# Performance work log

Measured on AMD Instinct MI355X. Metric: run time of the kernel, lower is better.

Reference implementation:

```python
import jax, jax.numpy as jnp
import numpy as np

B, S, D, H, DFF = 8, 1024, 1024, 16, 4096
DK = D // H
EPS = 1e-5


def setup_inputs() -> dict:
    key = jax.random.key(0)
    ks = jax.random.split(key, 12)
    sc = lambda n: 1.0 / np.sqrt(n)
    return {
        "x": jax.random.normal(ks[0], (B, S, D), jnp.float32),
        "src_mask": jnp.ones((B, 1, 1, S), jnp.int32),
        "wq": jax.random.normal(ks[1], (D, D), jnp.float32) * sc(D),
        "bq": jnp.zeros((D,), jnp.float32),
        "wk": jax.random.normal(ks[2], (D, D), jnp.float32) * sc(D),
        "bk": jnp.zeros((D,), jnp.float32),
        "wv": jax.random.normal(ks[3], (D, D), jnp.float32) * sc(D),
        "bv": jnp.zeros((D,), jnp.float32),
        "wo": jax.random.normal(ks[4], (D, D), jnp.float32) * sc(D),
        "bo": jnp.zeros((D,), jnp.float32),
        "w1": jax.random.normal(ks[5], (DFF, D), jnp.float32) * sc(D),
        "b1": jnp.zeros((DFF,), jnp.float32),
        "w2": jax.random.normal(ks[6], (D, DFF), jnp.float32) * sc(DFF),
        "b2": jnp.zeros((D,), jnp.float32),
        "g1": jnp.ones((1,), jnp.float32),
        "be1": jnp.zeros((1,), jnp.float32),
        "g2": jnp.ones((1,), jnp.float32),
        "be2": jnp.zeros((1,), jnp.float32),
    }


def _layernorm(x, gamma, beta):
    # Faithful to source: torch.var defaults to unbiased (ddof=1); scalar gamma/beta.
    mu = jnp.mean(x, axis=-1, keepdims=True)
    var = jnp.var(x, axis=-1, keepdims=True, ddof=1)
    return gamma * (x - mu) / jnp.sqrt(var + EPS) + beta


def _mha(x, wq, bq, wk, bk, wv, bv, wo, bo):
    q = (x @ wq.T + bq).reshape(B, S, H, DK).transpose(0, 2, 1, 3)
    k = (x @ wk.T + bk).reshape(B, S, H, DK).transpose(0, 2, 1, 3)
    v = (x @ wv.T + bv).reshape(B, S, H, DK).transpose(0, 2, 1, 3)
    scores = jnp.einsum("bhqd,bhkd->bhqk", q, k) / np.sqrt(DK)
    # NOTE: source uses non-inplace masked_fill whose result is discarded,
    # so the mask has no effect on the executed math; we replicate that.
    attn = jax.nn.softmax(scores, axis=-1)
    out = jnp.einsum("bhqk,bhkd->bhqd", attn, v)
    out = out.transpose(0, 2, 1, 3).reshape(B, S, D)
    return out @ wo.T + bo


def reference(x, src_mask, wq, bq, wk, bk, wv, bv, wo, bo,
              w1, b1, w2, b2, g1, be1, g2, be2):
    # residual 1: pre-norm self-attention (dropout=0 in eval)
    x = x + _mha(_layernorm(x, g1, be1), wq, bq, wk, bk, wv, bv, wo, bo)
    # residual 2: pre-norm FFN
    h = _layernorm(x, g2, be2)
    ff = jax.nn.relu(h @ w1.T + b1) @ w2.T + b2
    return x + ff
```

## Files before the change

kernel.cpp:

```cpp
#include <hip/hip_runtime.h>

typedef unsigned short u16;
typedef unsigned int u32;
typedef __attribute__((ext_vector_type(8))) __bf16 bf16x8;
typedef __attribute__((ext_vector_type(4))) float f32x4;

#define B_ 8
#define S_ 1024
#define D_ 1024
#define H_ 16
#define DK_ 64
#define DFF_ 4096
#define LDQKV 3072

__device__ __forceinline__ float bflo(u32 u) { return __uint_as_float(u << 16); }
__device__ __forceinline__ float bfhi(u32 u) { return __uint_as_float(u & 0xffff0000u); }
__device__ __forceinline__ u16 f2bf(float f) {
    u32 u = __float_as_uint(f);
    u += 0x7fffu + ((u >> 16) & 1u);
    return (u16)(u >> 16);
}

__device__ __forceinline__ void gl2lds16(const u16* g, u16* l) {
    __builtin_amdgcn_global_load_lds(
        (const __attribute__((address_space(1))) void*)g,
        (__attribute__((address_space(3))) void*)l, 16, 0, 0);
}

__global__ __launch_bounds__(256) void sniff_kernel(const u16* __restrict__ w,
                                                    int* __restrict__ flag) {
    float mx = 0.f;
    for (int i = threadIdx.x; i < 4096; i += 256) {
        float v = fabsf(bflo((u32)w[i]));
        if (!isnan(v)) mx = fmaxf(mx, v);
    }
#pragma unroll
    for (int m = 1; m < 64; m <<= 1) mx = fmaxf(mx, __shfl_xor(mx, m, 64));
    __shared__ float wmx[4];
    if ((threadIdx.x & 63) == 0) wmx[threadIdx.x >> 6] = mx;
    __syncthreads();
    if (threadIdx.x == 0) {
        float m2 = fmaxf(fmaxf(wmx[0], wmx[1]), fmaxf(wmx[2], wmx[3]));
        *flag = (m2 > 1e3f) ? 1 : 0;
    }
}

__global__ __launch_bounds__(256) void norm_kernel(const void* __restrict__ in,
                                                   u16* __restrict__ out, int n,
                                                   const int* __restrict__ flag) {
    const int i = blockIdx.x * 256 + threadIdx.x;
    if (i >= n) return;
    if (*flag)
        out[i] = f2bf(((const float*)in)[i]);
    else
        out[i] = ((const u16*)in)[i];
}

struct SmallTbl {
    const void* src[10];
    u16* dst[10];
    int n[10];
};
__global__ __launch_bounds__(256) void norm_small(SmallTbl tb,
                                                  const int* __restrict__ flag) {
    int i = blockIdx.x * 256 + threadIdx.x;
    const int f = *flag;
#pragma unroll
    for (int j = 0; j < 10; ++j) {
        if (i < tb.n[j]) {
            if (f)
                tb.dst[j][i] = f2bf(((const float*)tb.src[j])[i]);
            else
                tb.dst[j][i] = ((const u16*)tb.src[j])[i];
            return;
        }
        i -= tb.n[j];
    }
}

template <int INF32>
__global__ __launch_bounds__(256) void ln_kernel(const void* __restrict__ in,
                                                 const u16* __restrict__ gs,
                                                 const u16* __restrict__ bs,
                                                 u16* __restrict__ out) {
    const int row = blockIdx.x, t = threadIdx.x;
    float v0, v1, v2, v3;
    if (INF32) {
        const float* p = (const float*)in + (size_t)row * D_ + t * 4;
        float4 f = *(const float4*)p;
        v0 = f.x; v1 = f.y; v2 = f.z; v3 = f.w;
    } else {
        const u16* p = (const u16*)in + (size_t)row * D_ + t * 4;
        uint2 u = *(const uint2*)p;
        v0 = bflo(u.x); v1 = bfhi(u.x); v2 = bflo(u.y); v3 = bfhi(u.y);
    }
    float s = v0 + v1 + v2 + v3;
    float sq = v0 * v0 + v1 * v1 + v2 * v2 + v3 * v3;
#pragma unroll
    for (int m = 1; m < 64; m <<= 1) {
        s += __shfl_xor(s, m, 64);
        sq += __shfl_xor(sq, m, 64);
    }
    __shared__ float ss[4], sqs[4];
    const int w = t >> 6;
    if ((t & 63) == 0) { ss[w] = s; sqs[w] = sq; }
    __syncthreads();
    s = ss[0] + ss[1] + ss[2] + ss[3];
    sq = sqs[0] + sqs[1] + sqs[2] + sqs[3];
    const float mu = s * (1.f / 1024.f);
    float var = (sq - 1024.f * mu * mu) * (1.f / 1023.f);
    var = fmaxf(var, 0.f);
    const float rstd = rsqrtf(var + 1e-5f);
    const float gm = bflo((u32)gs[0]);
    const float bt = bflo((u32)bs[0]);
    const float y0 = gm * (v0 - mu) * rstd + bt;
    const float y1 = gm * (v1 - mu) * rstd + bt;
    const float y2 = gm * (v2 - mu) * rstd + bt;
    const float y3 = gm * (v3 - mu) * rstd + bt;
    uint2 uo;
    uo.x = (u32)f2bf(y0) | ((u32)f2bf(y1) << 16);
    uo.y = (u32)f2bf(y2) | ((u32)f2bf(y3) << 16);
    *(uint2*)(out + (size_t)row * D_ + t * 4) = uo;
}

template <int RELU, int RES, int OUTF>
__global__ __launch_bounds__(256, 2) void gemm_bt(const u16* __restrict__ A,
                                                  const u16* __restrict__ W,
                                                  const u16* __restrict__ bias,
                                                  const void* __restrict__ res,
                                                  void* __restrict__ out,
                                                  int M, int N, int K,
                                                  const int* __restrict__ oflag) {
    __shared__ __align__(16) u16 As[128 * 32];
    __shared__ __align__(16) u16 Bs[128 * 32];
    const int t = threadIdx.x;
    const int lane = t & 63, w = t >> 6;
    const int wm = w >> 1, wn = w & 1;
    const int m0 = blockIdx.y * 128, n0 = blockIdx.x * 128;

    f32x4 acc[4][4];
#pragma unroll
    for (int mi = 0; mi < 4; ++mi)
#pragma unroll
        for (int ni = 0; ni < 4; ++ni) acc[mi][ni] = (f32x4){0.f, 0.f, 0.f, 0.f};

    const int sr = lane >> 2, skc = lane & 3;
    const u16* Ag0 = A + (size_t)(m0 + w * 16 + sr) * K + skc * 8;
    const u16* Bg0 = W + (size_t)(n0 + w * 16 + sr) * K + skc * 8;
    const size_t h64 = (size_t)64 * K;
    u16* Asd0 = &As[(w * 16) * 32];
    u16* Asd1 = &As[(64 + w * 16) * 32];
    u16* Bsd0 = &Bs[(w * 16) * 32];
    u16* Bsd1 = &Bs[(64 + w * 16) * 32];

    const u16* As_r = &As[(wm * 64 + (lane & 15)) * 32 + (lane >> 4) * 8];
    const u16* Bs_r = &Bs[(wn * 64 + (lane & 15)) * 32 + (lane >> 4) * 8];

    for (int kt = 0; kt < K; kt += 32) {
        __syncthreads();
        gl2lds16(Ag0 + kt, Asd0);
        gl2lds16(Ag0 + h64 + kt, Asd1);
        gl2lds16(Bg0 + kt, Bsd0);
        gl2lds16(Bg0 + h64 + kt, Bsd1);
        __syncthreads();
        bf16x8 af[4], bfr[4];
#pragma unroll
        for (int i = 0; i < 4; ++i) {
            af[i] = *(const bf16x8*)(As_r + i * 16 * 32);
            bfr[i] = *(const bf16x8*)(Bs_r + i * 16 * 32);
        }
#pragma unroll
        for (int mi = 0; mi < 4; ++mi)
#pragma unroll
            for (int ni = 0; ni < 4; ++ni)
                acc[mi][ni] = __builtin_amdgcn_mfma_f32_16x16x32_bf16(af[mi], bfr[ni], acc[mi][ni], 0, 0, 0);
    }

    const bool f32o = (OUTF == 1) || (OUTF == 2 && oflag[0] != 0);
    const int qd = lane >> 4, cl = lane & 15;
#pragma unroll
    for (int ni = 0; ni < 4; ++ni) {
        const int col = n0 + wn * 64 + ni * 16 + cl;
        const float bv = bflo((u32)bias[col]);
#pragma unroll
        for (int mi = 0; mi < 4; ++mi) {
#pragma unroll
            for (int j = 0; j < 4; ++j) {
                const int row = m0 + wm * 64 + mi * 16 + qd * 4 + j;
                float vv = acc[mi][ni][j] + bv;
                if (RELU) vv = fmaxf(vv, 0.f);
                if (RES == 1) vv += bflo((u32)((const u16*)res)[(size_t)row * N + col]);
                if (RES == 2) vv += ((const float*)res)[(size_t)row * N + col];
                if (f32o)
                    ((float*)out)[(size_t)row * N + col] = vv;
                else
                    ((u16*)out)[(size_t)row * N + col] = f2bf(vv);
            }
        }
    }
}

__global__ __launch_bounds__(256, 2) void attn_mfma(const u16* __restrict__ QKV,
                                                    u16* __restrict__ O) {
    __shared__ __align__(16) u16 lds[6 * 64 * 72];
    u16* Ks = lds;
    u16* VsT = lds + 64 * 72;

    const int t = threadIdx.x;
    const int lane = t & 63, w = t >> 6;
    u16* Pw = lds + (2 + w) * 64 * 72;
    const int b = blockIdx.y >> 4, h = blockIdx.y & 15;
    const int q_base = blockIdx.x * 256 + w * 64;
    const int c = lane & 15, g = lane >> 4;
    const float SC = 0.18033688011112042f;

    bf16x8 qfrag[4][2];
#pragma unroll
    for (int ni = 0; ni < 4; ++ni)
#pragma unroll
        for (int kc = 0; kc < 2; ++kc)
            qfrag[ni][kc] = *(const bf16x8*)(QKV + (size_t)(b * S_ + q_base + 16 * ni + c) * LDQKV +
                                             h * 64 + kc * 32 + 8 * g);

    f32x4 acc_o[4][4];
#pragma unroll
    for (int mi = 0; mi < 4; ++mi)
#pragma unroll
        for (int ni = 0; ni < 4; ++ni) acc_o[mi][ni] = (f32x4){0.f, 0.f, 0.f, 0.f};
    float m_st[4] = {-1e30f, -1e30f, -1e30f, -1e30f};
    float l_st[4] = {0.f, 0.f, 0.f, 0.f};

    const size_t kbase = (size_t)(b * S_) * LDQKV + 1024 + h * 64;
    const size_t vbase = (size_t)(b * S_) * LDQKV + 2048 + h * 64;
    const int srow = t >> 2, sc4 = t & 3;

    for (int kt = 0; kt < 16; ++kt) {
        __syncthreads();
        {
            const u16* kp = QKV + kbase + (size_t)(kt * 64 + srow) * LDQKV + sc4 * 16;
            uint4 k0 = *(const uint4*)kp;
            uint4 k1 = *(const uint4*)(kp + 8);
            *(uint4*)&Ks[srow * 72 + sc4 * 16] = k0;
            *(uint4*)&Ks[srow * 72 + sc4 * 16 + 8] = k1;
            const u16* vp = QKV + vbase + (size_t)(kt * 64 + srow) * LDQKV + sc4 * 16;
            uint4 v0 = *(const uint4*)vp;
            uint4 v1 = *(const uint4*)(vp + 8);
            u32 vw[8] = {v0.x, v0.y, v0.z, v0.w, v1.x, v1.y, v1.z, v1.w};
#pragma unroll
            for (int i = 0; i < 8; ++i) {
                VsT[(sc4 * 16 + 2 * i) * 72 + srow] = (u16)(vw[i] & 0xffffu);
                VsT[(sc4 * 16 + 2 * i + 1) * 72 + srow] = (u16)(vw[i] >> 16);
            }
        }
        __syncthreads();

        f32x4 acc_s[4][4];
#pragma unroll
        for (int mi = 0; mi < 4; ++mi)
#pragma unroll
            for (int ni = 0; ni < 4; ++ni) acc_s[mi][ni] = (f32x4){0.f, 0.f, 0.f, 0.f};
#pragma unroll
        for (int kc = 0; kc < 2; ++kc) {
            bf16x8 kf[4];
#pragma unroll
            for (int mi = 0; mi < 4; ++mi)
                kf[mi] = *(const bf16x8*)&Ks[(16 * mi + c) * 72 + kc * 32 + 8 * g];
#pragma unroll
            for (int mi = 0; mi < 4; ++mi)
#pragma unroll
                for (int ni = 0; ni < 4; ++ni)
                    acc_s[mi][ni] = __builtin_amdgcn_mfma_f32_16x16x32_bf16(
                        kf[mi], qfrag[ni][kc], acc_s[mi][ni], 0, 0, 0);
        }

        float alpha[4];
#pragma unroll
        for (int ni = 0; ni < 4; ++ni) {
            float mx = -1e30f;
#pragma unroll
            for (int mi = 0; mi < 4; ++mi) {
#pragma unroll
                for (int j = 0; j < 4; ++j) {
                    acc_s[mi][ni][j] *= SC;
                    mx = fmaxf(mx, acc_s[mi][ni][j]);
                }
            }
            mx = fmaxf(mx, __shfl_xor(mx, 16, 64));
            mx = fmaxf(mx, __shfl_xor(mx, 32, 64));
            const float mn = fmaxf(m_st[ni], mx);
            alpha[ni] = exp2f(m_st[ni] - mn);
            m_st[ni] = mn;
            float sum = 0.f;
#pragma unroll
            for (int mi = 0; mi < 4; ++mi) {
                float p0 = exp2f(acc_s[mi][ni][0] - mn);
                float p1 = exp2f(acc_s[mi][ni][1] - mn);
                float p2 = exp2f(acc_s[mi][ni][2] - mn);
                float p3 = exp2f(acc_s[mi][ni][3] - mn);
                sum += (p0 + p1) + (p2 + p3);
                uint2 pk;
                pk.x = (u32)f2bf(p0) | ((u32)f2bf(p1) << 16);
                pk.y = (u32)f2bf(p2) | ((u32)f2bf(p3) << 16);
                *(uint2*)&Pw[(16 * ni + c) * 72 + 16 * mi + 4 * g] = pk;
            }
            sum += __shfl_xor(sum, 16, 64);
            sum += __shfl_xor(sum, 32, 64);
            l_st[ni] = l_st[ni] * alpha[ni] + sum;
        }
#pragma unroll
        for (int mi = 0; mi < 4; ++mi)
#pragma unroll
            for (int ni = 0; ni < 4; ++ni) {
#pragma unroll
                for (int j = 0; j < 4; ++j) acc_o[mi][ni][j] *= alpha[ni];
            }

#pragma unroll
        for (int kc = 0; kc < 2; ++kc) {
            bf16x8 vf[4], pf[4];
#pragma unroll
            for (int mi = 0; mi < 4; ++mi)
                vf[mi] = *(const bf16x8*)&VsT[(16 * mi + c) * 72 + kc * 32 + 8 * g];
#pragma unroll
            for (int ni = 0; ni < 4; ++ni)
                pf[ni] = *(const bf16x8*)&Pw[(16 * ni + c) * 72 + kc * 32 + 8 * g];
#pragma unroll
            for (int mi = 0; mi < 4; ++mi)
#pragma unroll
                for (int ni = 0; ni < 4; ++ni)
                    acc_o[mi][ni] = __builtin_amdgcn_mfma_f32_16x16x32_bf16(
                        vf[mi], pf[ni], acc_o[mi][ni], 0, 0, 0);
        }
    }

#pragma unroll
    for (int ni = 0; ni < 4; ++ni) {
        const float inv_l = 1.f / l_st[ni];
        u16* op = O + (size_t)(b * S_ + q_base + 16 * ni + c) * D_ + h * 64;
#pragma unroll
        for (int mi = 0; mi < 4; ++mi) {
            uint2 uo;
            uo.x = (u32)f2bf(acc_o[mi][ni][0] * inv_l) |
                   ((u32)f2bf(acc_o[mi][ni][1] * inv_l) << 16);
            uo.y = (u32)f2bf(acc_o[mi][ni][2] * inv_l) |
                   ((u32)f2bf(acc_o[mi][ni][3] * inv_l) << 16);
            *(uint2*)(op + 16 * mi + 4 * g) = uo;
        }
    }
}

extern "C" void kernel_launch(void* const* d_in, const int* in_sizes, int n_in,
                              void* d_out, int out_size, void* d_ws, size_t ws_size,
                              hipStream_t stream) {
    (void)in_sizes; (void)n_in; (void)out_size; (void)ws_size;
    char* ws = (char*)d_ws;
    const size_t MB = 1ull << 20;
    const size_t KB = 1024;
    u16* xn   = (u16*)(ws);
    u16* wqkv = (u16*)(ws + 16 * MB);
    u16* won  = (u16*)(ws + 22 * MB);
    u16* w1n  = (u16*)(ws + 24 * MB);
    u16* w2n  = (u16*)(ws + 32 * MB);
    u16* bqkv = (u16*)(ws + 40 * MB);
    u16* bon  = (u16*)(ws + 40 * MB + 64 * KB);
    u16* b1n  = (u16*)(ws + 40 * MB + 128 * KB);
    u16* b2n  = (u16*)(ws + 40 * MB + 192 * KB);
    u16* g1n  = (u16*)(ws + 40 * MB + 256 * KB);
    u16* be1n = (u16*)(ws + 40 * MB + 320 * KB);
    u16* g2n  = (u16*)(ws + 40 * MB + 384 * KB);
    u16* be2n = (u16*)(ws + 40 * MB + 448 * KB);
    int* flag = (int*)(ws + 40 * MB + 512 * KB);
    u16* h1   = (u16*)(ws + 48 * MB);
    u16* qkv  = (u16*)(ws + 64 * MB);
    float* x2 = (float*)(ws + 64 * MB);
    u16* h2   = (u16*)(ws + 96 * MB);
    u16* f1   = (u16*)(ws + 112 * MB);

    const int M = B_ * S_;

    sniff_kernel<<<1, 256, 0, stream>>>((const u16*)d_in[2], flag);
    auto nrm = [&](const void* in, u16* out, int n) {
        norm_kernel<<<(n + 255) / 256, 256, 0, stream>>>(in, out, n, flag);
    };
    nrm(d_in[0],  xn,  B_ * S_ * D_);
    nrm(d_in[2],  wqkv,               D_ * D_);
    nrm(d_in[4],  wqkv + D_ * D_,     D_ * D_);
    nrm(d_in[6],  wqkv + 2 * D_ * D_, D_ * D_);
    nrm(d_in[8],  won, D_ * D_);
    nrm(d_in[10], w1n, DFF_ * D_);
    nrm(d_in[12], w2n, D_ * DFF_);
    {
        SmallTbl tb;
        tb.src[0] = d_in[3];  tb.dst[0] = bqkv;        tb.n[0] = D_;
        tb.src[1] = d_in[5];  tb.dst[1] = bqkv + D_;   tb.n[1] = D_;
        tb.src[2] = d_in[7];  tb.dst[2] = bqkv + 2 * D_; tb.n[2] = D_;
        tb.src[3] = d_in[9];  tb.dst[3] = bon;         tb.n[3] = D_;
        tb.src[4] = d_in[11]; tb.dst[4] = b1n;         tb.n[4] = DFF_;
        tb.src[5] = d_in[13]; tb.dst[5] = b2n;         tb.n[5] = D_;
        tb.src[6] = d_in[14]; tb.dst[6] = g1n;         tb.n[6] = 1;
        tb.src[7] = d_in[15]; tb.dst[7] = be1n;        tb.n[7] = 1;
        tb.src[8] = d_in[16]; tb.dst[8] = g2n;         tb.n[8] = 1;
        tb.src[9] = d_in[17]; tb.dst[9] = be2n;        tb.n[9] = 1;
        const int tot = 5 * D_ + DFF_ + 4;
        norm_small<<<(tot + 255) / 256, 256, 0, stream>>>(tb, flag);
    }

    ln_kernel<0><<<M, 256, 0, stream>>>((const void*)xn, g1n, be1n, h1);
    gemm_bt<0, 0, 0><<<dim3(LDQKV / 128, M / 128), 256, 0, stream>>>(h1, wqkv, bqkv, nullptr, qkv, M, LDQKV, D_, nullptr);
    attn_mfma<<<dim3(S_ / 256, B_ * H_), 256, 0, stream>>>(qkv, h1);
    gemm_bt<0, 1, 1><<<dim3(D_ / 128, M / 128), 256, 0, stream>>>(h1, won, bon, (const void*)xn, x2, M, D_, D_, nullptr);
    ln_kernel<1><<<M, 256, 0, stream>>>((const void*)x2, g2n, be2n, h2);
    gemm_bt<1, 0, 0><<<dim3(DFF_ / 128, M / 128), 256, 0, stream>>>(h2, w1n, b1n, nullptr, f1, M, DFF_, D_, nullptr);
    gemm_bt<0, 2, 2><<<dim3(D_ / 128, M / 128), 256, 0, stream>>>(f1, w2n, b2n, (const void*)x2, (void*)d_out, M, D_, DFF_, flag);
}
```

Baseline: 588.6 us.

## Drop input conversion pass, swizzle GEMM LDS layout, and group tiles for L2

Removes the separate pass that converted x to bf16. LayerNorm and the out-projection residual now read the raw input directly, selecting f32 or bf16 at runtime from the dtype flag. The GEMM LDS layout gets an XOR swizzle of 16-byte chunks to cut bank conflicts on fragment reads. The 2D grid becomes a 1D grid with grouped tile ordering (8 M-tiles per group) to improve L2 reuse of weight tiles. The added flag checks cost a few extra branches, and the residual is now taken from the full-precision input.

After: 566.7 us. 1.04x faster.

```diff
diff --git a/kernel.cpp b/kernel.cpp
--- a/kernel.cpp
+++ b/kernel.cpp
@@ -78,14 +78,16 @@
     }
 }
 
-template <int INF32>
+template <int INF>
 __global__ __launch_bounds__(256) void ln_kernel(const void* __restrict__ in,
                                                  const u16* __restrict__ gs,
                                                  const u16* __restrict__ bs,
-                                                 u16* __restrict__ out) {
+                                                 u16* __restrict__ out,
+                                                 const int* __restrict__ flag) {
     const int row = blockIdx.x, t = threadIdx.x;
+    const bool f32in = (INF == 1) || (INF == 2 && flag[0] != 0);
     float v0, v1, v2, v3;
-    if (INF32) {
+    if (f32in) {
         const float* p = (const float*)in + (size_t)row * D_ + t * 4;
         float4 f = *(const float4*)p;
         v0 = f.x; v1 = f.y; v2 = f.z; v3 = f.w;
@@ -136,7 +138,14 @@
     const int t = threadIdx.x;
     const int lane = t & 63, w = t >> 6;
     const int wm = w >> 1, wn = w & 1;
-    const int m0 = blockIdx.y * 128, n0 = blockIdx.x * 128;
+
+    const int nx = N >> 7;
+    const int gsz = nx << 3;
+    const int id = blockIdx.x;
+    const int grp = id / gsz;
+    const int rem = id - grp * gsz;
+    const int m0 = ((grp << 3) + (rem & 7)) << 7;
+    const int n0 = (rem >> 3) << 7;
 
     f32x4 acc[4][4];
 #pragma unroll
@@ -144,17 +153,20 @@
 #pragma unroll
         for (int ni = 0; ni < 4; ++ni) acc[mi][ni] = (f32x4){0.f, 0.f, 0.f, 0.f};
 
-    const int sr = lane >> 2, skc = lane & 3;
-    const u16* Ag0 = A + (size_t)(m0 + w * 16 + sr) * K + skc * 8;
-    const u16* Bg0 = W + (size_t)(n0 + w * 16 + sr) * K + skc * 8;
+    const int sr = lane >> 2, sk = lane & 3;
+    const int skg = sk ^ (sr & 3) ^ ((sr >> 2) & 3);
+    const u16* Ag0 = A + (size_t)(m0 + w * 16 + sr) * K + skg * 8;
+    const u16* Bg0 = W + (size_t)(n0 + w * 16 + sr) * K + skg * 8;
     const size_t h64 = (size_t)64 * K;
     u16* Asd0 = &As[(w * 16) * 32];
     u16* Asd1 = &As[(64 + w * 16) * 32];
     u16* Bsd0 = &Bs[(w * 16) * 32];
     u16* Bsd1 = &Bs[(64 + w * 16) * 32];
 
-    const u16* As_r = &As[(wm * 64 + (lane & 15)) * 32 + (lane >> 4) * 8];
-    const u16* Bs_r = &Bs[(wn * 64 + (lane & 15)) * 32 + (lane >> 4) * 8];
+    const int c = lane & 15, g = lane >> 4;
+    const int swc = g ^ (c & 3) ^ ((c >> 2) & 3);
+    const u16* As_r = &As[(wm * 64 + c) * 32 + swc * 8];
+    const u16* Bs_r = &Bs[(wn * 64 + c) * 32 + swc * 8];
 
     for (int kt = 0; kt < K; kt += 32) {
         __syncthreads();
@@ -176,7 +188,8 @@
                 acc[mi][ni] = __builtin_amdgcn_mfma_f32_16x16x32_bf16(af[mi], bfr[ni], acc[mi][ni], 0, 0, 0);
     }
 
-    const bool f32o = (OUTF == 1) || (OUTF == 2 && oflag[0] != 0);
+    const int fl = oflag ? oflag[0] : 0;
+    const bool f32o = (OUTF == 1) || (OUTF == 2 && fl != 0);
     const int qd = lane >> 4, cl = lane & 15;
 #pragma unroll
     for (int ni = 0; ni < 4; ++ni) {
@@ -189,8 +202,13 @@
                 const int row = m0 + wm * 64 + mi * 16 + qd * 4 + j;
                 float vv = acc[mi][ni][j] + bv;
                 if (RELU) vv = fmaxf(vv, 0.f);
-                if (RES == 1) vv += bflo((u32)((const u16*)res)[(size_t)row * N + col]);
                 if (RES == 2) vv += ((const float*)res)[(size_t)row * N + col];
+                if (RES == 3) {
+                    if (fl)
+                        vv += ((const float*)res)[(size_t)row * N + col];
+                    else
+                        vv += bflo((u32)((const u16*)res)[(size_t)row * N + col]);
+                }
                 if (f32o)
                     ((float*)out)[(size_t)row * N + col] = vv;
                 else
@@ -356,7 +374,6 @@
     char* ws = (char*)d_ws;
     const size_t MB = 1ull << 20;
     const size_t KB = 1024;
-    u16* xn   = (u16*)(ws);
     u16* wqkv = (u16*)(ws + 16 * MB);
     u16* won  = (u16*)(ws + 22 * MB);
     u16* w1n  = (u16*)(ws + 24 * MB);
@@ -382,7 +399,6 @@
     auto nrm = [&](const void* in, u16* out, int n) {
         norm_kernel<<<(n + 255) / 256, 256, 0, stream>>>(in, out, n, flag);
     };
-    nrm(d_in[0],  xn,  B_ * S_ * D_);
     nrm(d_in[2],  wqkv,               D_ * D_);
     nrm(d_in[4],  wqkv + D_ * D_,     D_ * D_);
     nrm(d_in[6],  wqkv + 2 * D_ * D_, D_ * D_);
@@ -391,25 +407,25 @@
     nrm(d_in[12], w2n, D_ * DFF_);
     {
         SmallTbl tb;
-        tb.src[0] = d_in[3];  tb.dst[0] = bqkv;        tb.n[0] = D_;
-        tb.src[1] = d_in[5];  tb.dst[1] = bqkv + D_;   tb.n[1] = D_;
+        tb.src[0] = d_in[3];  tb.dst[0] = bqkv;          tb.n[0] = D_;
+        tb.src[1] = d_in[5];  tb.dst[1] = bqkv + D_;     tb.n[1] = D_;
         tb.src[2] = d_in[7];  tb.dst[2] = bqkv + 2 * D_; tb.n[2] = D_;
-        tb.src[3] = d_in[9];  tb.dst[3] = bon;         tb.n[3] = D_;
-        tb.src[4] = d_in[11]; tb.dst[4] = b1n;         tb.n[4] = DFF_;
-        tb.src[5] = d_in[13]; tb.dst[5] = b2n;         tb.n[5] = D_;
-        tb.src[6] = d_in[14]; tb.dst[6] = g1n;         tb.n[6] = 1;
-        tb.src[7] = d_in[15]; tb.dst[7] = be1n;        tb.n[7] = 1;
-        tb.src[8] = d_in[16]; tb.dst[8] = g2n;         tb.n[8] = 1;
-        tb.src[9] = d_in[17]; tb.dst[9] = be2n;        tb.n[9] = 1;
+        tb.src[3] = d_in[9];  tb.dst[3] = bon;           tb.n[3] = D_;
+        tb.src[4] = d_in[11]; tb.dst[4] = b1n;           tb.n[4] = DFF_;
+        tb.src[5] = d_in[13]; tb.dst[5] = b2n;           tb.n[5] = D_;
+        tb.src[6] = d_in[14]; tb.dst[6] = g1n;           tb.n[6] = 1;
+        tb.src[7] = d_in[15]; tb.dst[7] = be1n;          tb.n[7] = 1;
+        tb.src[8] = d_in[16]; tb.dst[8] = g2n;           tb.n[8] = 1;
+        tb.src[9] = d_in[17]; tb.dst[9] = be2n;          tb.n[9] = 1;
         const int tot = 5 * D_ + DFF_ + 4;
         norm_small<<<(tot + 255) / 256, 256, 0, stream>>>(tb, flag);
     }
 
-    ln_kernel<0><<<M, 256, 0, stream>>>((const void*)xn, g1n, be1n, h1);
-    gemm_bt<0, 0, 0><<<dim3(LDQKV / 128, M / 128), 256, 0, stream>>>(h1, wqkv, bqkv, nullptr, qkv, M, LDQKV, D_, nullptr);
+    ln_kernel<2><<<M, 256, 0, stream>>>(d_in[0], g1n, be1n, h1, flag);
+    gemm_bt<0, 0, 0><<<(LDQKV / 128) * (M / 128), 256, 0, stream>>>(h1, wqkv, bqkv, nullptr, qkv, M, LDQKV, D_, flag);
     attn_mfma<<<dim3(S_ / 256, B_ * H_), 256, 0, stream>>>(qkv, h1);
-    gemm_bt<0, 1, 1><<<dim3(D_ / 128, M / 128), 256, 0, stream>>>(h1, won, bon, (const void*)xn, x2, M, D_, D_, nullptr);
-    ln_kernel<1><<<M, 256, 0, stream>>>((const void*)x2, g2n, be2n, h2);
-    gemm_bt<1, 0, 0><<<dim3(DFF_ / 128, M / 128), 256, 0, stream>>>(h2, w1n, b1n, nullptr, f1, M, DFF_, D_, nullptr);
-    gemm_bt<0, 2, 2><<<dim3(D_ / 128, M / 128), 256, 0, stream>>>(f1, w2n, b2n, (const void*)x2, (void*)d_out, M, D_, DFF_, flag);
-}
+    gemm_bt<0, 3, 1><<<(D_ / 128) * (M / 128), 256, 0, stream>>>(h1, won, bon, d_in[0], x2, M, D_, D_, flag);
+    ln_kernel<1><<<M, 256, 0, stream>>>((const void*)x2, g2n, be2n, h2, flag);
+    gemm_bt<1, 0, 0><<<(DFF_ / 128) * (M / 128), 256, 0, stream>>>(h2, w1n, b1n, nullptr, f1, M, DFF_, D_, flag);
+    gemm_bt<0, 2, 2><<<(D_ / 128) * (M / 128), 256, 0, stream>>>(f1, w2n, b2n, (const void*)x2, (void*)d_out, M, D_, DFF_, flag);
+}
```
